# Kernel optimization log

Measured on AMD Instinct MI355X. Metric: run time of the kernel, lower is better.

Reference implementation:

```python
import jax, jax.numpy as jnp
import numpy as np

B, T, C, H = 2, 2048, 1024, 16
HD = C // H  # head dim = 64


def setup_inputs() -> dict:
    key = jax.random.key(0)
    ks = jax.random.split(key, 5)
    s = 1.0 / np.sqrt(C)
    return {
        "x": jax.random.normal(ks[0], (B, T, C), dtype=jnp.float32),
        "W_attn": jax.random.normal(ks[1], (3 * C, C), dtype=jnp.float32) * s,
        "b_attn": jax.random.normal(ks[2], (3 * C,), dtype=jnp.float32) * 0.02,
        "W_proj": jax.random.normal(ks[3], (C, C), dtype=jnp.float32) * s,
        "b_proj": jax.random.normal(ks[4], (C,), dtype=jnp.float32) * 0.02,
    }


def reference(x, W_attn, b_attn, W_proj, b_proj):
    Bx, Tx, Cx = x.shape
    # fused QKV projection (torch Linear: x @ W.T + b)
    qkv = x @ W_attn.T + b_attn                      # [B,T,3C]
    q, k, v = jnp.split(qkv, 3, axis=-1)
    # [B,T,C] -> [B,H,T,hd]
    q = q.reshape(Bx, Tx, H, HD).transpose(0, 2, 1, 3)
    k = k.reshape(Bx, Tx, H, HD).transpose(0, 2, 1, 3)
    v = v.reshape(Bx, Tx, H, HD).transpose(0, 2, 1, 3)
    scale = 1.0 / np.sqrt(HD)
    att = jnp.einsum('bhqd,bhkd->bhqk', q, k) * scale  # [B,H,T,T]
    causal = jnp.tril(jnp.ones((Tx, Tx), dtype=bool))
    att = jnp.where(causal[None, None], att, -jnp.inf)
    att = jax.nn.softmax(att, axis=-1)
    y = jnp.einsum('bhqk,bhkd->bhqd', att, v)          # [B,H,T,hd]
    y = y.transpose(0, 2, 1, 3).reshape(Bx, Tx, Cx)
    return y @ W_proj.T + b_proj
```

## Files before the change

### kernel.cpp

```cpp
#include <hip/hip_runtime.h>

typedef unsigned short ushort_t;
typedef __bf16 bf16x8 __attribute__((ext_vector_type(8)));
typedef float f32x4 __attribute__((ext_vector_type(4)));

__device__ inline ushort_t f2bf(float f) {
  unsigned int u = __builtin_bit_cast(unsigned int, f);
  u += 0x7fff + ((u >> 16) & 1);
  return (ushort_t)(u >> 16);
}

__device__ inline unsigned pk_bf(float a, float b) {
  unsigned ua = __builtin_bit_cast(unsigned, a);
  unsigned ub = __builtin_bit_cast(unsigned, b);
  ua += 0x7fff + ((ua >> 16) & 1);
  ub += 0x7fff + ((ub >> 16) & 1);
  return __builtin_amdgcn_perm(ub, ua, 0x07060302);
}

__device__ inline void async_ld16(const ushort_t* g, const ushort_t* l) {
  __builtin_amdgcn_global_load_lds(
      (const __attribute__((address_space(1))) void*)g,
      (__attribute__((address_space(3))) void*)l, 16, 0, 0);
}

__global__ void cvt4(const float* __restrict__ in, ushort_t* __restrict__ out, int n4) {
  int i = blockIdx.x * blockDim.x + threadIdx.x;
  if (i >= n4) return;
  float4 f = ((const float4*)in)[i];
  unsigned long long p = (unsigned long long)f2bf(f.x)
      | ((unsigned long long)f2bf(f.y) << 16)
      | ((unsigned long long)f2bf(f.z) << 32)
      | ((unsigned long long)f2bf(f.w) << 48);
  ((unsigned long long*)out)[i] = p;
}

template <int MODE>
__global__ __launch_bounds__(256) void gemm_bt(
    const ushort_t* __restrict__ A, const ushort_t* __restrict__ B,
    const float* __restrict__ bias, float* __restrict__ Cf,
    ushort_t* __restrict__ Cb, ushort_t* __restrict__ vtb,
    int M, int N, int K, int ldc, float qscale) {
  __shared__ ushort_t As[128 * 32];
  __shared__ ushort_t Bs[128 * 32];
  const int tid = threadIdx.x;
  const int wave = tid >> 6, lane = tid & 63;
  const int quad = lane >> 4, l16 = lane & 15;
  const int m0 = blockIdx.y * 128, n0 = blockIdx.x * 128;
  const int wm = (wave >> 1) * 64, wn = (wave & 1) * 64;
  const ushort_t* Ag = A + (size_t)m0 * K;
  const ushort_t* Bg = B + (size_t)n0 * K;
  f32x4 acc[4][4] = {};

  for (int k0 = 0; k0 < K; k0 += 32) {
#pragma unroll
    for (int c = 0; c < 2; ++c) {
      int ci = c * 256 + tid;
      int r = ci >> 2, cc = ci & 3;
      int ldsoff = (c * 256 + wave * 64) * 8;
      async_ld16(Ag + (size_t)r * K + k0 + cc * 8, As + ldsoff);
      async_ld16(Bg + (size_t)r * K + k0 + cc * 8, Bs + ldsoff);
    }
    __syncthreads();
    bf16x8 af[4], bfr[4];
#pragma unroll
    for (int i = 0; i < 4; ++i) {
      af[i]  = *(const bf16x8*)(As + (wm + i * 16 + l16) * 32 + quad * 8);
      bfr[i] = *(const bf16x8*)(Bs + (wn + i * 16 + l16) * 32 + quad * 8);
    }
#pragma unroll
    for (int i = 0; i < 4; ++i)
#pragma unroll
      for (int j = 0; j < 4; ++j)
        acc[i][j] = __builtin_amdgcn_mfma_f32_16x16x32_bf16(af[i], bfr[j], acc[i][j], 0, 0, 0);
    __syncthreads();
  }

  if (MODE == 1 && n0 >= 2048) {
#pragma unroll
    for (int j = 0; j < 4; ++j) {
      int col = n0 + wn + j * 16 + l16;
      int cv = col - 2048;
      float bv = bias[col];
      size_t rowbase = ((size_t)(cv >> 6)) * 64 + (cv & 63);
#pragma unroll
      for (int i = 0; i < 4; ++i) {
        int rowb = m0 + wm + i * 16 + quad * 4;
        int bb = rowb >> 11, t = rowb & 2047;
        uint2 pp;
        pp.x = pk_bf(acc[i][j][0] + bv, acc[i][j][1] + bv);
        pp.y = pk_bf(acc[i][j][2] + bv, acc[i][j][3] + bv);
        *(uint2*)(vtb + (((size_t)bb * 1024 + rowbase) * 2048 + t)) = pp;
      }
    }
    return;
  }
#pragma unroll
  for (int j = 0; j < 4; ++j) {
    int col = n0 + wn + j * 16 + l16;
    float bv = bias[col];
    float sc = (MODE == 1 && col < 1024) ? qscale : 1.0f;
#pragma unroll
    for (int i = 0; i < 4; ++i)
#pragma unroll
      for (int r = 0; r < 4; ++r) {
        int row = m0 + wm + i * 16 + quad * 4 + r;
        float v = (acc[i][j][r] + bv) * sc;
        if (MODE == 1)
          Cb[(size_t)row * ldc + col] = f2bf(v);
        else
          Cf[(size_t)row * ldc + col] = v;
      }
  }
}

__global__ __launch_bounds__(256) void flash2(
    const ushort_t* __restrict__ qk, const ushort_t* __restrict__ vt,
    ushort_t* __restrict__ y) {
  __shared__ __align__(16) ushort_t Kb[2][4096];
  __shared__ __align__(16) ushort_t Vb[2][4096];
  __shared__ __align__(16) ushort_t Ps[64 * 72];
  const int tid = threadIdx.x, wave = tid >> 6, lane = tid & 63;
  const int quad = lane >> 4, l16 = lane & 15;
  const int r7 = l16 & 7;
  const int p = blockIdx.x, bh = blockIdx.y;
  const int b = bh >> 4, h = bh & 15;
  const int bT = b * 2048;
  const int qtA = 31 - p, qtB = p;

#pragma unroll
  for (int i = 0; i < 2; ++i) {
    int ci = i * 256 + tid;
    int row = ci >> 3;
    int chunk = (ci & 7) ^ (row & 7);
    ushort_t* lk = Kb[0] + (i * 256 + wave * 64) * 8;
    ushort_t* lv = Vb[0] + (i * 256 + wave * 64) * 8;
    async_ld16(qk + (size_t)(bT + qtA * 64 + row) * 2048 + h * 64 + chunk * 8, lk);
    async_ld16(qk + (size_t)(bT + qtB * 64 + row) * 2048 + h * 64 + chunk * 8, lv);
  }
  __syncthreads();
  bf16x8 qaA[2], qaB[2];
#pragma unroll
  for (int ks = 0; ks < 2; ++ks) {
    int off = (wave * 16 + l16) * 64 + (((ks * 4 + quad) ^ r7) * 8);
    qaA[ks] = *(const bf16x8*)(Kb[0] + off);
    qaB[ks] = *(const bf16x8*)(Vb[0] + off);
  }
  __syncthreads();

  f32x4 oA[4] = {}, oB[4] = {};
  float mA = -1e30f, lA = 0.f, mB = -1e30f, lB = 0.f;

  auto stage = [&](int kt, int bsel) {
    int k0 = kt * 64;
#pragma unroll
    for (int i = 0; i < 2; ++i) {
      int ci = i * 256 + tid;
      int row = ci >> 3;
      int chunk = (ci & 7) ^ (row & 7);
      ushort_t* lk = Kb[bsel] + (i * 256 + wave * 64) * 8;
      ushort_t* lv = Vb[bsel] + (i * 256 + wave * 64) * 8;
      async_ld16(qk + (size_t)(bT + k0 + row) * 2048 + 1024 + h * 64 + chunk * 8, lk);
      async_ld16(vt + (size_t)(bh * 64 + row) * 2048 + k0 + chunk * 8, lv);
    }
  };

  auto process = [&](const bf16x8* qa, f32x4* o, float& m, float& l, bool diag,
                     const ushort_t* Kc, const ushort_t* Vc) {
    f32x4 s[4] = {};
#pragma unroll
    for (int ks = 0; ks < 2; ++ks) {
      bf16x8 qf = qa[ks];
#pragma unroll
      for (int j = 0; j < 4; ++j) {
        bf16x8 kf = *(const bf16x8*)(Kc + (j * 16 + l16) * 64 + (((ks * 4 + quad) ^ r7) * 8));
        s[j] = __builtin_amdgcn_mfma_f32_16x16x32_bf16(kf, qf, s[j], 0, 0, 0);
      }
    }
    if (diag) {
      int qloc = wave * 16 + l16;
#pragma unroll
      for (int j = 0; j < 4; ++j)
#pragma unroll
        for (int r = 0; r < 4; ++r)
          if (j * 16 + quad * 4 + r > qloc) s[j][r] = -1e30f;
    }
    float vmax = -1e30f;
#pragma unroll
    for (int j = 0; j < 4; ++j)
#pragma unroll
      for (int r = 0; r < 4; ++r) vmax = fmaxf(vmax, s[j][r]);
    vmax = fmaxf(vmax, __shfl_xor(vmax, 16, 64));
    vmax = fmaxf(vmax, __shfl_xor(vmax, 32, 64));
    float mn = fmaxf(m, vmax);
    float al = __expf(m - mn);
    m = mn;
    float rs = 0.f;
#pragma unroll
    for (int j = 0; j < 4; ++j)
#pragma unroll
      for (int r = 0; r < 4; ++r) {
        float pv = __expf(s[j][r] - mn);
        s[j][r] = pv;
        rs += pv;
      }
    rs += __shfl_xor(rs, 16, 64);
    rs += __shfl_xor(rs, 32, 64);
    l = l * al + rs;
#pragma unroll
    for (int j = 0; j < 4; ++j) {
      uint2 pp;
      pp.x = pk_bf(s[j][0], s[j][1]);
      pp.y = pk_bf(s[j][2], s[j][3]);
      *(uint2*)(Ps + (wave * 16 + l16) * 72 + j * 16 + quad * 4) = pp;
    }
    __builtin_amdgcn_s_waitcnt(0xc07f);
#pragma unroll
    for (int j = 0; j < 4; ++j)
#pragma unroll
      for (int r = 0; r < 4; ++r) o[j][r] *= al;
#pragma unroll
    for (int ks = 0; ks < 2; ++ks) {
      bf16x8 pf = *(const bf16x8*)(Ps + (wave * 16 + l16) * 72 + ks * 32 + quad * 8);
#pragma unroll
      for (int j = 0; j < 4; ++j) {
        bf16x8 vf = *(const bf16x8*)(Vc + (j * 16 + l16) * 64 + (((ks * 4 + quad) ^ r7) * 8));
        o[j] = __builtin_amdgcn_mfma_f32_16x16x32_bf16(vf, pf, o[j], 0, 0, 0);
      }
    }
  };

  stage(0, 0);
  const int KT = qtA + 1;
  for (int kt = 0; kt < KT; ++kt) {
    const int cur = kt & 1;
    __syncthreads();
    if (kt + 1 < KT) stage(kt + 1, cur ^ 1);
    const ushort_t* Kc = Kb[cur];
    const ushort_t* Vc = Vb[cur];
    process(qaA, oA, mA, lA, kt == qtA, Kc, Vc);
    if (kt <= qtB) process(qaB, oB, mB, lB, kt == qtB, Kc, Vc);
  }

  auto wrt = [&](int qt, f32x4* o, float l) {
    float inv = 1.f / l;
    size_t row = (size_t)(bT + qt * 64 + wave * 16 + l16);
#pragma unroll
    for (int j = 0; j < 4; ++j) {
      uint2 pp;
      pp.x = pk_bf(o[j][0] * inv, o[j][1] * inv);
      pp.y = pk_bf(o[j][2] * inv, o[j][3] * inv);
      *(uint2*)(y + row * 1024 + h * 64 + j * 16 + quad * 4) = pp;
    }
  };
  wrt(qtA, oA, lA);
  wrt(qtB, oB, lB);
}

extern "C" void kernel_launch(void* const* d_in, const int* in_sizes, int n_in,
                              void* d_out, int out_size, void* d_ws, size_t ws_size,
                              hipStream_t stream) {
  const float* x  = (const float*)d_in[0];
  const float* Wa = (const float*)d_in[1];
  const float* ba = (const float*)d_in[2];
  const float* Wp = (const float*)d_in[3];
  const float* bp = (const float*)d_in[4];
  float* out = (float*)d_out;
  char* ws = (char*)d_ws;
  ushort_t* xb  = (ushort_t*)(ws);
  ushort_t* Wab = (ushort_t*)(ws + 8388608);
  ushort_t* Wpb = (ushort_t*)(ws + 14680064);
  ushort_t* qkb = (ushort_t*)(ws + 16777216);
  ushort_t* yb  = (ushort_t*)(ws + 33554432);
  ushort_t* vtb = (ushort_t*)(ws + 41943040);

  cvt4<<<4096 * 1024 / 4 / 256, 256, 0, stream>>>(x, xb, 4096 * 1024 / 4);
  cvt4<<<3072 * 1024 / 4 / 256, 256, 0, stream>>>(Wa, Wab, 3072 * 1024 / 4);
  cvt4<<<1024 * 1024 / 4 / 256, 256, 0, stream>>>(Wp, Wpb, 1024 * 1024 / 4);
  gemm_bt<1><<<dim3(24, 32), 256, 0, stream>>>(
      xb, Wab, ba, nullptr, qkb, vtb, 4096, 3072, 1024, 2048, 0.125f);
  flash2<<<dim3(16, 32), 256, 0, stream>>>(qkb, vtb, yb);
  gemm_bt<0><<<dim3(8, 32), 256, 0, stream>>>(
      yb, Wpb, bp, out, nullptr, nullptr, 4096, 1024, 1024, 1024, 1.0f);
}
```

Before: 220.6 us.

## Template GEMM tiles with K=64 swizzled LDS, split flash blocks, use exp2

The GEMM is now templated on block and warp tile sizes. It loads K=64 per iteration into XOR-swizzled LDS to cut bank conflicts and barrier count, and the output projection uses 64x128 tiles so more blocks launch. The attention kernel no longer pairs two query tiles per block to balance causal work; it launches one block per query tile and relies on the scheduler to balance the uneven causal work. Softmax switches to exp2f with log2(e) folded into the Q scale. Together these trade load balance and Q reuse for more parallelism and fewer instructions.

After: 246.1 us. +11.6%, slower.

```diff
diff --git a/kernel.cpp b/kernel.cpp
--- a/kernel.cpp
+++ b/kernel.cpp
@@ -35,56 +35,67 @@
   ((unsigned long long*)out)[i] = p;
 }
 
-template <int MODE>
+template <int BM, int BN, int IM, int JN, int MODE>
 __global__ __launch_bounds__(256) void gemm_bt(
     const ushort_t* __restrict__ A, const ushort_t* __restrict__ B,
     const float* __restrict__ bias, float* __restrict__ Cf,
     ushort_t* __restrict__ Cb, ushort_t* __restrict__ vtb,
     int M, int N, int K, int ldc, float qscale) {
-  __shared__ ushort_t As[128 * 32];
-  __shared__ ushort_t Bs[128 * 32];
+  constexpr int NWN = BN / (JN * 16);
+  __shared__ __align__(16) ushort_t As[BM * 64];
+  __shared__ __align__(16) ushort_t Bs[BN * 64];
   const int tid = threadIdx.x;
   const int wave = tid >> 6, lane = tid & 63;
   const int quad = lane >> 4, l16 = lane & 15;
-  const int m0 = blockIdx.y * 128, n0 = blockIdx.x * 128;
-  const int wm = (wave >> 1) * 64, wn = (wave & 1) * 64;
+  const int r7 = l16 & 7;
+  const int wr = wave / NWN, wc = wave % NWN;
+  const int wm = wr * IM * 16, wn = wc * JN * 16;
+  const int m0 = blockIdx.y * BM, n0 = blockIdx.x * BN;
   const ushort_t* Ag = A + (size_t)m0 * K;
   const ushort_t* Bg = B + (size_t)n0 * K;
-  f32x4 acc[4][4] = {};
-
-  for (int k0 = 0; k0 < K; k0 += 32) {
-#pragma unroll
-    for (int c = 0; c < 2; ++c) {
-      int ci = c * 256 + tid;
-      int r = ci >> 2, cc = ci & 3;
-      int ldsoff = (c * 256 + wave * 64) * 8;
-      async_ld16(Ag + (size_t)r * K + k0 + cc * 8, As + ldsoff);
-      async_ld16(Bg + (size_t)r * K + k0 + cc * 8, Bs + ldsoff);
+  f32x4 acc[IM][JN] = {};
+
+  for (int k0 = 0; k0 < K; k0 += 64) {
+#pragma unroll
+    for (int p = 0; p < BM / 32; ++p) {
+      int ci = p * 256 + tid;
+      int row = ci >> 3, ch = (ci & 7) ^ (row & 7);
+      async_ld16(Ag + (size_t)row * K + k0 + ch * 8, As + (p * 256 + wave * 64) * 8);
+    }
+#pragma unroll
+    for (int p = 0; p < BN / 32; ++p) {
+      int ci = p * 256 + tid;
+      int row = ci >> 3, ch = (ci & 7) ^ (row & 7);
+      async_ld16(Bg + (size_t)row * K + k0 + ch * 8, Bs + (p * 256 + wave * 64) * 8);
     }
     __syncthreads();
-    bf16x8 af[4], bfr[4];
-#pragma unroll
-    for (int i = 0; i < 4; ++i) {
-      af[i]  = *(const bf16x8*)(As + (wm + i * 16 + l16) * 32 + quad * 8);
-      bfr[i] = *(const bf16x8*)(Bs + (wn + i * 16 + l16) * 32 + quad * 8);
-    }
-#pragma unroll
-    for (int i = 0; i < 4; ++i)
-#pragma unroll
-      for (int j = 0; j < 4; ++j)
-        acc[i][j] = __builtin_amdgcn_mfma_f32_16x16x32_bf16(af[i], bfr[j], acc[i][j], 0, 0, 0);
+#pragma unroll
+    for (int ks = 0; ks < 2; ++ks) {
+      bf16x8 af[IM], bfr[JN];
+#pragma unroll
+      for (int i = 0; i < IM; ++i)
+        af[i] = *(const bf16x8*)(As + (wm + i * 16 + l16) * 64 + (((ks * 4 + quad) ^ r7) * 8));
+#pragma unroll
+      for (int j = 0; j < JN; ++j)
+        bfr[j] = *(const bf16x8*)(Bs + (wn + j * 16 + l16) * 64 + (((ks * 4 + quad) ^ r7) * 8));
+#pragma unroll
+      for (int i = 0; i < IM; ++i)
+#pragma unroll
+        for (int j = 0; j < JN; ++j)
+          acc[i][j] = __builtin_amdgcn_mfma_f32_16x16x32_bf16(af[i], bfr[j], acc[i][j], 0, 0, 0);
+    }
     __syncthreads();
   }
 
   if (MODE == 1 && n0 >= 2048) {
 #pragma unroll
-    for (int j = 0; j < 4; ++j) {
+    for (int j = 0; j < JN; ++j) {
       int col = n0 + wn + j * 16 + l16;
       int cv = col - 2048;
       float bv = bias[col];
       size_t rowbase = ((size_t)(cv >> 6)) * 64 + (cv & 63);
 #pragma unroll
-      for (int i = 0; i < 4; ++i) {
+      for (int i = 0; i < IM; ++i) {
         int rowb = m0 + wm + i * 16 + quad * 4;
         int bb = rowb >> 11, t = rowb & 2047;
         uint2 pp;
@@ -96,12 +107,12 @@
     return;
   }
 #pragma unroll
-  for (int j = 0; j < 4; ++j) {
+  for (int j = 0; j < JN; ++j) {
     int col = n0 + wn + j * 16 + l16;
     float bv = bias[col];
     float sc = (MODE == 1 && col < 1024) ? qscale : 1.0f;
 #pragma unroll
-    for (int i = 0; i < 4; ++i)
+    for (int i = 0; i < IM; ++i)
 #pragma unroll
       for (int r = 0; r < 4; ++r) {
         int row = m0 + wm + i * 16 + quad * 4 + r;
@@ -123,50 +134,48 @@
   const int tid = threadIdx.x, wave = tid >> 6, lane = tid & 63;
   const int quad = lane >> 4, l16 = lane & 15;
   const int r7 = l16 & 7;
-  const int p = blockIdx.x, bh = blockIdx.y;
+  const int qt = 31 - blockIdx.x;
+  const int bh = blockIdx.y;
   const int b = bh >> 4, h = bh & 15;
   const int bT = b * 2048;
-  const int qtA = 31 - p, qtB = p;
 
 #pragma unroll
   for (int i = 0; i < 2; ++i) {
     int ci = i * 256 + tid;
-    int row = ci >> 3;
-    int chunk = (ci & 7) ^ (row & 7);
-    ushort_t* lk = Kb[0] + (i * 256 + wave * 64) * 8;
-    ushort_t* lv = Vb[0] + (i * 256 + wave * 64) * 8;
-    async_ld16(qk + (size_t)(bT + qtA * 64 + row) * 2048 + h * 64 + chunk * 8, lk);
-    async_ld16(qk + (size_t)(bT + qtB * 64 + row) * 2048 + h * 64 + chunk * 8, lv);
+    int row = ci >> 3, ch = (ci & 7) ^ (row & 7);
+    async_ld16(qk + (size_t)(bT + qt * 64 + row) * 2048 + h * 64 + ch * 8,
+               Kb[0] + (i * 256 + wave * 64) * 8);
   }
   __syncthreads();
-  bf16x8 qaA[2], qaB[2];
-#pragma unroll
-  for (int ks = 0; ks < 2; ++ks) {
-    int off = (wave * 16 + l16) * 64 + (((ks * 4 + quad) ^ r7) * 8);
-    qaA[ks] = *(const bf16x8*)(Kb[0] + off);
-    qaB[ks] = *(const bf16x8*)(Vb[0] + off);
-  }
+  bf16x8 qa[2];
+#pragma unroll
+  for (int ks = 0; ks < 2; ++ks)
+    qa[ks] = *(const bf16x8*)(Kb[0] + (wave * 16 + l16) * 64 + (((ks * 4 + quad) ^ r7) * 8));
   __syncthreads();
 
-  f32x4 oA[4] = {}, oB[4] = {};
-  float mA = -1e30f, lA = 0.f, mB = -1e30f, lB = 0.f;
+  f32x4 o[4] = {};
+  float m = -1e30f, l = 0.f;
 
   auto stage = [&](int kt, int bsel) {
     int k0 = kt * 64;
 #pragma unroll
     for (int i = 0; i < 2; ++i) {
       int ci = i * 256 + tid;
-      int row = ci >> 3;
-      int chunk = (ci & 7) ^ (row & 7);
-      ushort_t* lk = Kb[bsel] + (i * 256 + wave * 64) * 8;
-      ushort_t* lv = Vb[bsel] + (i * 256 + wave * 64) * 8;
-      async_ld16(qk + (size_t)(bT + k0 + row) * 2048 + 1024 + h * 64 + chunk * 8, lk);
-      async_ld16(vt + (size_t)(bh * 64 + row) * 2048 + k0 + chunk * 8, lv);
+      int row = ci >> 3, ch = (ci & 7) ^ (row & 7);
+      async_ld16(qk + (size_t)(bT + k0 + row) * 2048 + 1024 + h * 64 + ch * 8,
+                 Kb[bsel] + (i * 256 + wave * 64) * 8);
+      async_ld16(vt + (size_t)(bh * 64 + row) * 2048 + k0 + ch * 8,
+                 Vb[bsel] + (i * 256 + wave * 64) * 8);
     }
   };
 
-  auto process = [&](const bf16x8* qa, f32x4* o, float& m, float& l, bool diag,
-                     const ushort_t* Kc, const ushort_t* Vc) {
+  stage(0, 0);
+  for (int kt = 0; kt <= qt; ++kt) {
+    const int cur = kt & 1;
+    __syncthreads();
+    if (kt < qt) stage(kt + 1, cur ^ 1);
+    const ushort_t* Kc = Kb[cur];
+    const ushort_t* Vc = Vb[cur];
     f32x4 s[4] = {};
 #pragma unroll
     for (int ks = 0; ks < 2; ++ks) {
@@ -177,7 +186,7 @@
         s[j] = __builtin_amdgcn_mfma_f32_16x16x32_bf16(kf, qf, s[j], 0, 0, 0);
       }
     }
-    if (diag) {
+    if (kt == qt) {
       int qloc = wave * 16 + l16;
 #pragma unroll
       for (int j = 0; j < 4; ++j)
@@ -193,14 +202,14 @@
     vmax = fmaxf(vmax, __shfl_xor(vmax, 16, 64));
     vmax = fmaxf(vmax, __shfl_xor(vmax, 32, 64));
     float mn = fmaxf(m, vmax);
-    float al = __expf(m - mn);
+    float al = exp2f(m - mn);
     m = mn;
     float rs = 0.f;
 #pragma unroll
     for (int j = 0; j < 4; ++j)
 #pragma unroll
       for (int r = 0; r < 4; ++r) {
-        float pv = __expf(s[j][r] - mn);
+        float pv = exp2f(s[j][r] - mn);
         s[j][r] = pv;
         rs += pv;
       }
@@ -228,33 +237,17 @@
         o[j] = __builtin_amdgcn_mfma_f32_16x16x32_bf16(vf, pf, o[j], 0, 0, 0);
       }
     }
-  };
-
-  stage(0, 0);
-  const int KT = qtA + 1;
-  for (int kt = 0; kt < KT; ++kt) {
-    const int cur = kt & 1;
-    __syncthreads();
-    if (kt + 1 < KT) stage(kt + 1, cur ^ 1);
-    const ushort_t* Kc = Kb[cur];
-    const ushort_t* Vc = Vb[cur];
-    process(qaA, oA, mA, lA, kt == qtA, Kc, Vc);
-    if (kt <= qtB) process(qaB, oB, mB, lB, kt == qtB, Kc, Vc);
-  }
-
-  auto wrt = [&](int qt, f32x4* o, float l) {
-    float inv = 1.f / l;
-    size_t row = (size_t)(bT + qt * 64 + wave * 16 + l16);
-#pragma unroll
-    for (int j = 0; j < 4; ++j) {
-      uint2 pp;
-      pp.x = pk_bf(o[j][0] * inv, o[j][1] * inv);
-      pp.y = pk_bf(o[j][2] * inv, o[j][3] * inv);
-      *(uint2*)(y + row * 1024 + h * 64 + j * 16 + quad * 4) = pp;
-    }
-  };
-  wrt(qtA, oA, lA);
-  wrt(qtB, oB, lB);
+  }
+
+  float inv = 1.f / l;
+  size_t row = (size_t)(bT + qt * 64 + wave * 16 + l16);
+#pragma unroll
+  for (int j = 0; j < 4; ++j) {
+    uint2 pp;
+    pp.x = pk_bf(o[j][0] * inv, o[j][1] * inv);
+    pp.y = pk_bf(o[j][2] * inv, o[j][3] * inv);
+    *(uint2*)(y + row * 1024 + h * 64 + j * 16 + quad * 4) = pp;
+  }
 }
 
 extern "C" void kernel_launch(void* const* d_in, const int* in_sizes, int n_in,
@@ -277,9 +270,9 @@
   cvt4<<<4096 * 1024 / 4 / 256, 256, 0, stream>>>(x, xb, 4096 * 1024 / 4);
   cvt4<<<3072 * 1024 / 4 / 256, 256, 0, stream>>>(Wa, Wab, 3072 * 1024 / 4);
   cvt4<<<1024 * 1024 / 4 / 256, 256, 0, stream>>>(Wp, Wpb, 1024 * 1024 / 4);
-  gemm_bt<1><<<dim3(24, 32), 256, 0, stream>>>(
-      xb, Wab, ba, nullptr, qkb, vtb, 4096, 3072, 1024, 2048, 0.125f);
-  flash2<<<dim3(16, 32), 256, 0, stream>>>(qkb, vtb, yb);
-  gemm_bt<0><<<dim3(8, 32), 256, 0, stream>>>(
+  gemm_bt<128, 128, 4, 4, 1><<<dim3(24, 32), 256, 0, stream>>>(
+      xb, Wab, ba, nullptr, qkb, vtb, 4096, 3072, 1024, 2048, 0.18033688011112042f);
+  flash2<<<dim3(32, 32), 256, 0, stream>>>(qkb, vtb, yb);
+  gemm_bt<64, 128, 4, 2, 0><<<dim3(8, 64), 256, 0, stream>>>(
       yb, Wpb, bp, out, nullptr, nullptr, 4096, 1024, 1024, 1024, 1.0f);
 }
```
